# Kernel tuning notes

Measured on AMD Instinct MI355X. Metric: run time of the kernel, lower is better.

The kernel has to match this reference:

```python
import jax, jax.numpy as jnp
import numpy as np

B = 1 << 20  # batch rows
H = 2        # LSTM input_size = hidden_size = 2
K = 11       # number of parallel LSTMs
C = 34       # classifier input size (11*2 + 12 others)
C15 = 51     # int(34 * 1.5)
P = 5        # toPredict_size


def setup_inputs() -> dict:
    key = jax.random.key(0)
    ks = jax.random.split(key, 12)
    s = 0.1
    inp = {
        "input_data": jax.random.normal(ks[0], (B, C), dtype=jnp.float32),
        # Per-LSTM input->gates weights, PyTorch gate order (i, f, g, o): [K, 4H, H]
        "W_ih": jax.random.normal(ks[1], (K, 4 * H, H), dtype=jnp.float32) * s,
        "b_ih": jax.random.normal(ks[2], (K, 4 * H), dtype=jnp.float32) * s,
        # h0 = 0 so W_hh contributes nothing; only its bias b_hh matters.
        "b_hh": jax.random.normal(ks[3], (K, 4 * H), dtype=jnp.float32) * s,
        "W1": jax.random.normal(ks[4], (C15, C), dtype=jnp.float32) * s,
        "b1": jax.random.normal(ks[5], (C15,), dtype=jnp.float32) * s,
        "W2": jax.random.normal(ks[6], (C15, C15), dtype=jnp.float32) * s,
        "b2": jax.random.normal(ks[7], (C15,), dtype=jnp.float32) * s,
        "W3": jax.random.normal(ks[8], (C, C15), dtype=jnp.float32) * s,
        "b3": jax.random.normal(ks[9], (C,), dtype=jnp.float32) * s,
        "W4": jax.random.normal(ks[10], (P, C), dtype=jnp.float32) * s,
        "b4": jax.random.normal(ks[11], (P,), dtype=jnp.float32) * s,
    }
    return inp


def _lstm_heads(x, W_ih, b_ih, b_hh):
    # x: [B, K, H]; single-step LSTM from zero state for each of K heads.
    gates = jnp.einsum("bkh,kgh->bkg", x, W_ih) + b_ih + b_hh  # [B, K, 4H]
    i, f, g, o = jnp.split(gates, 4, axis=-1)  # each [B, K, H]
    c = jax.nn.sigmoid(i) * jnp.tanh(g)        # f*c0 = 0 since c0 = 0
    h = jax.nn.sigmoid(o) * jnp.tanh(c)
    return h  # [B, K, H]


def reference(input_data, W_ih, b_ih, b_hh, W1, b1, W2, b2, W3, b3, W4, b4):
    bsz = input_data.shape[0]
    x_seqs = input_data[:, : K * H].reshape(bsz, K, H)
    others = input_data[:, K * H :]  # [B, 12]
    h = _lstm_heads(x_seqs, W_ih, b_ih, b_hh).reshape(bsz, K * H)
    cated = jnp.concatenate([h, others], axis=-1)  # [B, 34]
    z = jax.nn.relu(cated @ W1.T + b1)
    z = jax.nn.relu(z @ W2.T + b2)
    z = jax.nn.relu(z @ W3.T + b3)
    out = jax.nn.sigmoid(z @ W4.T + b4)  # [B, 5]
    return out
```

## Files before the change

### kernel.cpp

```cpp
#include <hip/hip_runtime.h>


#define BLK  256
#define WPB  4
#define KSEQ 11

typedef _Float16 h2   __attribute__((ext_vector_type(2)));
typedef _Float16 h8   __attribute__((ext_vector_type(8)));
typedef float    f4   __attribute__((ext_vector_type(4)));
typedef unsigned u16v __attribute__((ext_vector_type(16)));

struct __attribute__((packed, aligned(8))) pf4 { f4 v; };

#define N_FRAG_U32 6144
#define N_BIAS     3072
#define N_LSTM     288

__device__ __align__(16) float    g_lstm[N_LSTM];
__device__ __align__(16) unsigned g_frag[N_FRAG_U32];
__device__ __align__(16) float    g_bias[N_BIAS];

__device__ __forceinline__ h2 pk(float a, float b) {
    auto r = __builtin_amdgcn_cvt_pkrtz(a, b);
    union { decltype(r) f; h2 h; } c; c.f = r; return c.h;
}
__device__ __forceinline__ unsigned as_u32(h2 h) {
    union { h2 h; unsigned u; } c; c.h = h; return c.u;
}
__device__ __forceinline__ float uf(unsigned u) {
    union { unsigned u; float f; } c; c.u = u; return c.f;
}
__device__ __forceinline__ unsigned pkrelu(float a, float b) {
    h2 p = pk(a, b);
    h2 z = {(_Float16)0.0f, (_Float16)0.0f};
    h2 r = __builtin_elementwise_max(p, z);
    return as_u32(r);
}
__device__ __forceinline__ float fast_exp(float x) {
#if __has_builtin(__builtin_amdgcn_exp2f)
    return __builtin_amdgcn_exp2f(x * 1.44269504088896340736f);
#else
    return __expf(x);
#endif
}
__device__ __forceinline__ float fast_rcp(float x) {
#if __has_builtin(__builtin_amdgcn_rcpf)
    return __builtin_amdgcn_rcpf(x);
#else
    return 1.0f / x;
#endif
}
__device__ __forceinline__ float sig1(float x)  { return fast_rcp(1.0f + fast_exp(-x)); }

__device__ __forceinline__ float sigtanh(float a, float b) {
    float ea = fast_exp(-a);
    float eb = fast_exp(2.0f * b);
    return (eb - 1.0f) * fast_rcp((1.0f + ea) * (eb + 1.0f));
}

__device__ __forceinline__ void sload3(const unsigned* p, u16v& c0, u16v& c1, u16v& c2) {
    asm volatile("s_load_dwordx16 %0, %3, 0x0\n\t"
                 "s_load_dwordx16 %1, %3, 0x40\n\t"
                 "s_load_dwordx16 %2, %3, 0x80\n\t"
                 "s_waitcnt lgkmcnt(0)"
                 : "=&s"(c0), "=&s"(c1), "=&s"(c2) : "s"(p));
}
__device__ __forceinline__ unsigned pick48(const u16v& c0, const u16v& c1, const u16v& c2, int j) {
    return j < 16 ? c0[j] : (j < 32 ? c1[j - 16] : c2[j - 32]);
}

__device__ __forceinline__ void lstm_one(const u16v& c0, const u16v& c1, const u16v& c2, int base,
                                         float2 x, h2& outp)
{
    float w0  = uf(pick48(c0, c1, c2, base + 0)),  w1  = uf(pick48(c0, c1, c2, base + 1));
    float w2  = uf(pick48(c0, c1, c2, base + 2)),  w3  = uf(pick48(c0, c1, c2, base + 3));
    float w8  = uf(pick48(c0, c1, c2, base + 8)),  w9  = uf(pick48(c0, c1, c2, base + 9));
    float w10 = uf(pick48(c0, c1, c2, base + 10)), w11 = uf(pick48(c0, c1, c2, base + 11));
    float w12 = uf(pick48(c0, c1, c2, base + 12)), w13 = uf(pick48(c0, c1, c2, base + 13));
    float w14 = uf(pick48(c0, c1, c2, base + 14)), w15 = uf(pick48(c0, c1, c2, base + 15));
    float B0  = uf(pick48(c0, c1, c2, base + 16)), B1v = uf(pick48(c0, c1, c2, base + 17));
    float B4  = uf(pick48(c0, c1, c2, base + 20)), B5  = uf(pick48(c0, c1, c2, base + 21));
    float B6  = uf(pick48(c0, c1, c2, base + 22)), B7  = uf(pick48(c0, c1, c2, base + 23));

    float x0 = x.x, x1 = x.y;
    float gi0 = B0  + x0 * w0  + x1 * w1;
    float gi1 = B1v + x0 * w2  + x1 * w3;
    float gg0 = B4  + x0 * w8  + x1 * w9;
    float gg1 = B5  + x0 * w10 + x1 * w11;
    float go0 = B6  + x0 * w12 + x1 * w13;
    float go1 = B7  + x0 * w14 + x1 * w15;
    float cc0 = sigtanh(gi0, gg0);
    float cc1 = sigtanh(gi1, gg1);
    float h0  = sigtanh(go0, cc0);
    float h1  = sigtanh(go1, cc1);
    outp = pk(h0, h1);
}

__global__ void prep_weights(const float* __restrict__ W_ih, const float* __restrict__ b_ih,
                             const float* __restrict__ b_hh,
                             const float* __restrict__ W1, const float* __restrict__ b1,
                             const float* __restrict__ W2, const float* __restrict__ b2,
                             const float* __restrict__ W3, const float* __restrict__ b3,
                             const float* __restrict__ W4, const float* __restrict__ b4)
{
    const int gid = blockIdx.x * blockDim.x + threadIdx.x;
    const int gs  = gridDim.x * blockDim.x;

    for (int i = gid; i < N_FRAG_U32; i += gs) {
        int t = i >> 8, rlo = i & 255;
        int lane = rlo >> 2, j = rlo & 3;
        const float* W; int N, K, ld, ks, nt;
        if (t < 8)       { W = W1; N = 51; K = 34; ld = 34; ks = t >> 2;     nt = t & 3; }
        else if (t < 16) { W = W2; N = 51; K = 51; ld = 51; ks = (t-8) >> 2; nt = (t-8) & 3; }
        else if (t < 22) { W = W3; N = 34; K = 51; ld = 51; ks = (t-16) / 3; nt = (t-16) % 3; }
        else             { W = W4; N = 5;  K = 34; ld = 34; ks = t - 22;     nt = 0; }
        int m = nt * 16 + (lane & 15);
        int k_lo, k_hi;
        if (t < 8) {
            int p = ks * 16 + (lane >> 4) * 4 + j;
            k_lo = 2 * p; k_hi = k_lo + 1;
        } else {
            int q = ks * 32 + (lane >> 4) * 8 + 2 * j;
            k_lo = (2 * (q >> 5) + ((q & 7) >> 2)) * 16 + ((q >> 3) & 3) * 4 + (q & 3);
            int q1 = q + 1;
            k_hi = (2 * (q1 >> 5) + ((q1 & 7) >> 2)) * 16 + ((q1 >> 3) & 3) * 4 + (q1 & 3);
        }
        float a = (m < N && k_lo < K) ? W[m * ld + k_lo] : 0.f;
        float b = (m < N && k_hi < K) ? W[m * ld + k_hi] : 0.f;
        g_frag[i] = as_u32(pk(a, b));
    }
    for (int i = gid; i < N_BIAS; i += gs) {
        int bt = i >> 8, rem = i & 255;
        int lane = rem >> 2, r = rem & 3;
        const float* bv; int N, ot;
        if (bt < 4)       { bv = b1; N = 51; ot = bt; }
        else if (bt < 8)  { bv = b2; N = 51; ot = bt - 4; }
        else if (bt < 11) { bv = b3; N = 34; ot = bt - 8; }
        else              { bv = b4; N = 5;  ot = 0; }
        int n = ot * 16 + (lane >> 4) * 4 + r;
        g_bias[i] = (n < N) ? bv[n] : 0.f;
    }
    for (int i = gid; i < N_LSTM; i += gs) {
        int k = i / 24, cc = i - k * 24;
        float v = 0.f;
        if (k < KSEQ) v = (cc < 16) ? W_ih[k * 16 + cc]
                                    : b_ih[k * 8 + (cc - 16)] + b_hh[k * 8 + (cc - 16)];
        g_lstm[i] = v;
    }
}

__device__ __forceinline__ h8 load_frag(int tile, int l) {
    union { uint4 u; h8 h; } u;
    u.u = *(const uint4*)&g_frag[tile * 256 + l * 4];
    return u.h;
}

__device__ __forceinline__ void read_bfrags(h8 (&bf)[4][2], const unsigned* my, int l)
{
    const int c = l & 15, g = l >> 4;
    const int mrd = (c & 7) << 2;
    #pragma unroll
    for (int st = 0; st < 4; ++st)
      #pragma unroll
      for (int ks = 0; ks < 2; ++ks) {
        int idx = (st * 16 + c) * 32 + ((ks * 16 + g * 4) ^ mrd);
        union { uint4 u; h8 h; } u;
        u.u = *(const uint4*)&my[idx];
        bf[st][ks] = u.h;
      }
}

template<int NT, int TBASE, int BBASE>
__device__ __forceinline__ void layer_swapped(const h8 (&bf)[4][2], f4 (&acc)[4][4], int l)
{
    #pragma unroll
    for (int ot = 0; ot < NT; ++ot) {
        f4 bias4 = *(const f4*)&g_bias[(BBASE + ot) * 256 + l * 4];
        h8 af = load_frag(TBASE + ot, l);
        #pragma unroll
        for (int st = 0; st < 4; ++st)
          acc[ot][st] = __builtin_amdgcn_mfma_f32_16x16x32_f16(af, bf[st][0], bias4, 0, 0, 0);
    }
    #pragma unroll
    for (int ot = 0; ot < NT; ++ot) {
        h8 af = load_frag(TBASE + NT + ot, l);
        #pragma unroll
        for (int st = 0; st < 4; ++st)
          acc[ot][st] = __builtin_amdgcn_mfma_f32_16x16x32_f16(af, bf[st][1], acc[ot][st], 0, 0, 0);
    }
}

template<int NT>
__device__ __forceinline__ void pack_bfrags(const f4 (&acc)[4][4], h8 (&bf)[4][2])
{
    #pragma unroll
    for (int st = 0; st < 4; ++st)
      #pragma unroll
      for (int ks = 0; ks < 2; ++ks) {
        const int o0 = 2 * ks, o1 = 2 * ks + 1;
        union { unsigned u[4]; h8 h; } cvt;
        cvt.u[0] = pkrelu(acc[o0][st][0], acc[o0][st][1]);
        cvt.u[1] = pkrelu(acc[o0][st][2], acc[o0][st][3]);
        if (o1 < NT) {
            cvt.u[2] = pkrelu(acc[o1][st][0], acc[o1][st][1]);
            cvt.u[3] = pkrelu(acc[o1][st][2], acc[o1][st][3]);
        } else {
            cvt.u[2] = 0u; cvt.u[3] = 0u;
        }
        bf[st][ks] = cvt.h;
      }
}

__device__ __forceinline__ void stage0(const unsigned (&cp)[32], unsigned* my, int l)
{
    const int m = (l & 7) << 2;
    #pragma unroll
    for (int ch = 0; ch < 8; ++ch) {
        uint4 q = make_uint4(cp[4*ch], cp[4*ch+1], cp[4*ch+2], cp[4*ch+3]);
        *(uint4*)&my[l * 32 + ((4 * ch) ^ m)] = q;
    }
}

__global__ __launch_bounds__(BLK, 3)
void fused_rnn_mlp(const float* __restrict__ in, float* __restrict__ out, int nrows)
{
    __shared__ unsigned act[WPB * 2048];
    const int tid = threadIdx.x;
    const int w = tid >> 6, l = tid & 63;
    unsigned* my = &act[w * 2048];
    const long long rb = (long long)blockIdx.x * BLK;
    if (rb + BLK > nrows) return;
    const long long rw = rb + w * 64;

    float2 x[17];
    {
        const float* rp = in + (rw + l) * 34;
        #pragma unroll
        for (int q = 0; q < 8; ++q) {
            f4 v = ((const pf4*)(rp))[q].v;
            x[2 * q]     = make_float2(v.x, v.y);
            x[2 * q + 1] = make_float2(v.z, v.w);
        }
        x[16] = *(const float2*)(rp + 32);
    }

    unsigned cp[32];
    #pragma unroll
    for (int kp = 0; kp < 6; ++kp) {
        u16v c0, c1, c2;
        sload3((const unsigned*)&g_lstm[kp * 48], c0, c1, c2);
        h2 h;
        lstm_one(c0, c1, c2, 0, x[2 * kp], h);
        cp[2 * kp] = as_u32(h);
        if (kp < 5) {
            lstm_one(c0, c1, c2, 24, x[2 * kp + 1], h);
            cp[2 * kp + 1] = as_u32(h);
        }
    }
    #pragma unroll
    for (int t = 0; t < 6; ++t) cp[11 + t] = as_u32(pk(x[11 + t].x, x[11 + t].y));
    #pragma unroll
    for (int t = 17; t < 32; ++t) cp[t] = 0u;

    stage0(cp, my, l);

    h8 bf[4][2];
    f4 acc[4][4];

    read_bfrags(bf, my, l);
    layer_swapped<4, 0, 0>(bf, acc, l);
    pack_bfrags<4>(acc, bf);
    layer_swapped<4, 8, 4>(bf, acc, l);
    pack_bfrags<4>(acc, bf);
    layer_swapped<3, 16, 8>(bf, acc, l);
    pack_bfrags<3>(acc, bf);
    layer_swapped<1, 22, 11>(bf, acc, l);

    {
        const int c = l & 15, g = l >> 4;
        float* po = (float*)my;
        #pragma unroll
        for (int st = 0; st < 4; ++st) {
            const int sample = st * 16 + c;
            #pragma unroll
            for (int r = 0; r < 4; ++r) {
                int n = g * 4 + r;
                if (n < 5) po[sample * 9 + n] = acc[0][st][r];
            }
        }
    }

    {
        const float* po = (const float*)my;
        const long long ob = rw * 5;
        #pragma unroll
        for (int it = 0; it < 5; ++it) {
            int F   = it * 64 + l;
            int row = (F * 52429) >> 18;
            int cc  = F - row * 5;
            out[ob + F] = sig1(po[row * 9 + cc]);
        }
    }
}

extern "C" void kernel_launch(void* const* d_in, const int* in_sizes, int n_in,
                              void* d_out, int out_size, void* d_ws, size_t ws_size,
                              hipStream_t stream)
{
    const float* input = (const float*)d_in[0];
    const float* W_ih  = (const float*)d_in[1];
    const float* b_ih  = (const float*)d_in[2];
    const float* b_hh  = (const float*)d_in[3];
    const float* W1    = (const float*)d_in[4];
    const float* b1    = (const float*)d_in[5];
    const float* W2    = (const float*)d_in[6];
    const float* b2    = (const float*)d_in[7];
    const float* W3    = (const float*)d_in[8];
    const float* b3    = (const float*)d_in[9];
    const float* W4    = (const float*)d_in[10];
    const float* b4    = (const float*)d_in[11];
    float* out = (float*)d_out;

    int nrows = in_sizes[0] / 34;
    int grid  = nrows / BLK;

    hipLaunchKernelGGL(prep_weights, dim3(8), dim3(256), 0, stream,
                       W_ih, b_ih, b_hh, W1, b1, W2, b2, W3, b3, W4, b4);
    hipLaunchKernelGGL(fused_rnn_mlp, dim3(grid), dim3(BLK), 0, stream,
                       input, out, nrows);
}
```

Before: 53.02 us.

## Compute LSTM gate preactivations with MFMA and process samples in two halves

The per-head LSTM gate dot products, previously done with scalar FMAs using weights loaded into SGPRs, are moved into an augmented 112-row MFMA layer. That layer also passes the 12 extra features through an identity block. The first MLP layer's fragment mapping is permuted to match the new packed hidden layout. The wave's 64 samples are now processed in two halves of 32 to cut accumulator register pressure. This trades scalar VALU work for extra MFMA work, which mostly multiplies zeros, and sends the LSTM inputs through fp16 before the gate math, which may reduce accuracy.

```diff
diff --git a/kernel.cpp b/kernel.cpp
--- a/kernel.cpp
+++ b/kernel.cpp
@@ -3,20 +3,27 @@
 
 #define BLK  256
 #define WPB  4
-#define KSEQ 11
-
-typedef _Float16 h2   __attribute__((ext_vector_type(2)));
-typedef _Float16 h8   __attribute__((ext_vector_type(8)));
-typedef float    f4   __attribute__((ext_vector_type(4)));
-typedef unsigned u16v __attribute__((ext_vector_type(16)));
+
+#define N_FRAG_U32 (38 * 256)
+#define N_BIAS     (19 * 256)
+
+#define TB_G  0
+#define TB_L1 14
+#define TB_L2 22
+#define TB_L3 30
+#define TB_L4 36
+#define BB_L1 0
+#define BB_L2 4
+#define BB_L3 8
+#define BB_L4 11
+#define BB_G  12
+
+typedef _Float16 h2 __attribute__((ext_vector_type(2)));
+typedef _Float16 h8 __attribute__((ext_vector_type(8)));
+typedef float    f4 __attribute__((ext_vector_type(4)));
 
 struct __attribute__((packed, aligned(8))) pf4 { f4 v; };
 
-#define N_FRAG_U32 6144
-#define N_BIAS     3072
-#define N_LSTM     288
-
-__device__ __align__(16) float    g_lstm[N_LSTM];
 __device__ __align__(16) unsigned g_frag[N_FRAG_U32];
 __device__ __align__(16) float    g_bias[N_BIAS];
 
@@ -50,50 +57,43 @@
     return 1.0f / x;
 #endif
 }
-__device__ __forceinline__ float sig1(float x)  { return fast_rcp(1.0f + fast_exp(-x)); }
-
+__device__ __forceinline__ float sig1(float x) { return fast_rcp(1.0f + fast_exp(-x)); }
 __device__ __forceinline__ float sigtanh(float a, float b) {
     float ea = fast_exp(-a);
     float eb = fast_exp(2.0f * b);
     return (eb - 1.0f) * fast_rcp((1.0f + ea) * (eb + 1.0f));
 }
 
-__device__ __forceinline__ void sload3(const unsigned* p, u16v& c0, u16v& c1, u16v& c2) {
-    asm volatile("s_load_dwordx16 %0, %3, 0x0\n\t"
-                 "s_load_dwordx16 %1, %3, 0x40\n\t"
-                 "s_load_dwordx16 %2, %3, 0x80\n\t"
-                 "s_waitcnt lgkmcnt(0)"
-                 : "=&s"(c0), "=&s"(c1), "=&s"(c2) : "s"(p));
-}
-__device__ __forceinline__ unsigned pick48(const u16v& c0, const u16v& c1, const u16v& c2, int j) {
-    return j < 16 ? c0[j] : (j < 32 ? c1[j - 16] : c2[j - 32]);
-}
-
-__device__ __forceinline__ void lstm_one(const u16v& c0, const u16v& c1, const u16v& c2, int base,
-                                         float2 x, h2& outp)
-{
-    float w0  = uf(pick48(c0, c1, c2, base + 0)),  w1  = uf(pick48(c0, c1, c2, base + 1));
-    float w2  = uf(pick48(c0, c1, c2, base + 2)),  w3  = uf(pick48(c0, c1, c2, base + 3));
-    float w8  = uf(pick48(c0, c1, c2, base + 8)),  w9  = uf(pick48(c0, c1, c2, base + 9));
-    float w10 = uf(pick48(c0, c1, c2, base + 10)), w11 = uf(pick48(c0, c1, c2, base + 11));
-    float w12 = uf(pick48(c0, c1, c2, base + 12)), w13 = uf(pick48(c0, c1, c2, base + 13));
-    float w14 = uf(pick48(c0, c1, c2, base + 14)), w15 = uf(pick48(c0, c1, c2, base + 15));
-    float B0  = uf(pick48(c0, c1, c2, base + 16)), B1v = uf(pick48(c0, c1, c2, base + 17));
-    float B4  = uf(pick48(c0, c1, c2, base + 20)), B5  = uf(pick48(c0, c1, c2, base + 21));
-    float B6  = uf(pick48(c0, c1, c2, base + 22)), B7  = uf(pick48(c0, c1, c2, base + 23));
-
-    float x0 = x.x, x1 = x.y;
-    float gi0 = B0  + x0 * w0  + x1 * w1;
-    float gi1 = B1v + x0 * w2  + x1 * w3;
-    float gg0 = B4  + x0 * w8  + x1 * w9;
-    float gg1 = B5  + x0 * w10 + x1 * w11;
-    float go0 = B6  + x0 * w12 + x1 * w13;
-    float go1 = B7  + x0 * w14 + x1 * w15;
-    float cc0 = sigtanh(gi0, gg0);
-    float cc1 = sigtanh(gi1, gg1);
-    float h0  = sigtanh(go0, cc0);
-    float h1  = sigtanh(go1, cc1);
-    outp = pk(h0, h1);
+__device__ __forceinline__ int pi_map(int q) {
+    return (2 * (q >> 5) + ((q & 7) >> 2)) * 16 + ((q >> 3) & 3) * 4 + (q & 3);
+}
+__device__ __forceinline__ int phi_map(int q) {
+    int ksq = q >> 5, rem = q & 31, gq = rem >> 3, jj = rem & 7;
+    if (ksq == 0) {
+        if (jj < 6) { int u = 4 * jj + gq; return (u < 22) ? u : -1; }
+        return (gq < 3) ? (22 + 4 * gq + (jj - 6)) : -1;
+    }
+    if (jj < 2 && gq < 3) return 24 + 4 * gq + jj;
+    return -1;
+}
+__device__ __forceinline__ float waug(int row, int feat, const float* W_ih) {
+    if (feat >= 34) return 0.f;
+    if (row >= 96) { int cf = row - 96; return (cf < 12 && feat == 22 + cf) ? 1.f : 0.f; }
+    int u = row >> 2, r = row & 3;
+    if (u >= 22 || r == 3) return 0.f;
+    int k = u >> 1, jg = u & 1;
+    if ((feat >> 1) != k) return 0.f;
+    int h = feat & 1;
+    int g8 = (r == 0) ? jg : (r == 1) ? 4 + jg : 6 + jg;
+    return W_ih[k * 16 + g8 * 2 + h];
+}
+__device__ __forceinline__ float baug(int row, const float* b_ih, const float* b_hh) {
+    if (row >= 96) return 0.f;
+    int u = row >> 2, r = row & 3;
+    if (u >= 22 || r == 3) return 0.f;
+    int k = u >> 1, jg = u & 1;
+    int g8 = (r == 0) ? jg : (r == 1) ? 4 + jg : 6 + jg;
+    return b_ih[k * 8 + g8] + b_hh[k * 8 + g8];
 }
 
 __global__ void prep_weights(const float* __restrict__ W_ih, const float* __restrict__ b_ih,
@@ -109,43 +109,51 @@
     for (int i = gid; i < N_FRAG_U32; i += gs) {
         int t = i >> 8, rlo = i & 255;
         int lane = rlo >> 2, j = rlo & 3;
-        const float* W; int N, K, ld, ks, nt;
-        if (t < 8)       { W = W1; N = 51; K = 34; ld = 34; ks = t >> 2;     nt = t & 3; }
-        else if (t < 16) { W = W2; N = 51; K = 51; ld = 51; ks = (t-8) >> 2; nt = (t-8) & 3; }
-        else if (t < 22) { W = W3; N = 34; K = 51; ld = 51; ks = (t-16) / 3; nt = (t-16) % 3; }
-        else             { W = W4; N = 5;  K = 34; ld = 34; ks = t - 22;     nt = 0; }
-        int m = nt * 16 + (lane & 15);
-        int k_lo, k_hi;
-        if (t < 8) {
+        float a, b;
+        if (t < TB_L1) {
+            int ks = t / 7, ot = t - ks * 7;
+            int row = ot * 16 + (lane & 15);
             int p = ks * 16 + (lane >> 4) * 4 + j;
-            k_lo = 2 * p; k_hi = k_lo + 1;
+            a = waug(row, 2 * p,     W_ih);
+            b = waug(row, 2 * p + 1, W_ih);
         } else {
-            int q = ks * 32 + (lane >> 4) * 8 + 2 * j;
-            k_lo = (2 * (q >> 5) + ((q & 7) >> 2)) * 16 + ((q >> 3) & 3) * 4 + (q & 3);
-            int q1 = q + 1;
-            k_hi = (2 * (q1 >> 5) + ((q1 & 7) >> 2)) * 16 + ((q1 >> 3) & 3) * 4 + (q1 & 3);
-        }
-        float a = (m < N && k_lo < K) ? W[m * ld + k_lo] : 0.f;
-        float b = (m < N && k_hi < K) ? W[m * ld + k_hi] : 0.f;
+            const float* W; int N, K, ld, ks, nt, usephi;
+            if (t < TB_L2)      { W = W1; N = 51; K = 34; ld = 34; int tt = t - TB_L1; ks = tt >> 2; nt = tt & 3; usephi = 1; }
+            else if (t < TB_L3) { W = W2; N = 51; K = 51; ld = 51; int tt = t - TB_L2; ks = tt >> 2; nt = tt & 3; usephi = 0; }
+            else if (t < TB_L4) { W = W3; N = 34; K = 51; ld = 51; int tt = t - TB_L3; ks = tt / 3; nt = tt - 3 * ks; usephi = 0; }
+            else                { W = W4; N = 5;  K = 34; ld = 34; ks = t - TB_L4; nt = 0; usephi = 0; }
+            int m  = nt * 16 + (lane & 15);
+            int q0 = ks * 32 + (lane >> 4) * 8 + 2 * j;
+            int f0, f1;
+            if (usephi) { f0 = phi_map(q0); f1 = phi_map(q0 + 1); }
+            else {
+                f0 = pi_map(q0);     if (f0 >= K) f0 = -1;
+                f1 = pi_map(q0 + 1); if (f1 >= K) f1 = -1;
+            }
+            a = (m < N && f0 >= 0) ? W[m * ld + f0] : 0.f;
+            b = (m < N && f1 >= 0) ? W[m * ld + f1] : 0.f;
+        }
         g_frag[i] = as_u32(pk(a, b));
     }
+
     for (int i = gid; i < N_BIAS; i += gs) {
         int bt = i >> 8, rem = i & 255;
         int lane = rem >> 2, r = rem & 3;
-        const float* bv; int N, ot;
-        if (bt < 4)       { bv = b1; N = 51; ot = bt; }
-        else if (bt < 8)  { bv = b2; N = 51; ot = bt - 4; }
-        else if (bt < 11) { bv = b3; N = 34; ot = bt - 8; }
-        else              { bv = b4; N = 5;  ot = 0; }
-        int n = ot * 16 + (lane >> 4) * 4 + r;
-        g_bias[i] = (n < N) ? bv[n] : 0.f;
-    }
-    for (int i = gid; i < N_LSTM; i += gs) {
-        int k = i / 24, cc = i - k * 24;
-        float v = 0.f;
-        if (k < KSEQ) v = (cc < 16) ? W_ih[k * 16 + cc]
-                                    : b_ih[k * 8 + (cc - 16)] + b_hh[k * 8 + (cc - 16)];
-        g_lstm[i] = v;
+        int rowloc = (lane >> 4) * 4 + r;
+        float v;
+        if (bt < BB_G) {
+            const float* bv; int N, ot;
+            if (bt < 4)       { bv = b1; N = 51; ot = bt; }
+            else if (bt < 8)  { bv = b2; N = 51; ot = bt - 4; }
+            else if (bt < 11) { bv = b3; N = 34; ot = bt - 8; }
+            else              { bv = b4; N = 5;  ot = 0; }
+            int n = ot * 16 + rowloc;
+            v = (n < N) ? bv[n] : 0.f;
+        } else {
+            int row = (bt - BB_G) * 16 + rowloc;
+            v = baug(row, b_ih, b_hh);
+        }
+        g_bias[i] = v;
     }
 }
 
@@ -155,46 +163,77 @@
     return u.h;
 }
 
-__device__ __forceinline__ void read_bfrags(h8 (&bf)[4][2], const unsigned* my, int l)
-{
+__device__ __forceinline__ void read_bfrags2(h8 (&bf)[2][2], const unsigned* my, int l, int half) {
     const int c = l & 15, g = l >> 4;
     const int mrd = (c & 7) << 2;
     #pragma unroll
-    for (int st = 0; st < 4; ++st)
+    for (int st = 0; st < 2; ++st)
       #pragma unroll
       for (int ks = 0; ks < 2; ++ks) {
-        int idx = (st * 16 + c) * 32 + ((ks * 16 + g * 4) ^ mrd);
+        int idx = ((half * 2 + st) * 16 + c) * 32 + ((ks * 16 + g * 4) ^ mrd);
         union { uint4 u; h8 h; } u;
         u.u = *(const uint4*)&my[idx];
         bf[st][ks] = u.h;
       }
 }
 
+__device__ __forceinline__ void layer_gates(const h8 (&bf)[2][2], f4 (&acc)[7][2], int l) {
+    #pragma unroll
+    for (int ot = 0; ot < 7; ++ot) {
+        f4 bias4 = *(const f4*)&g_bias[(BB_G + ot) * 256 + l * 4];
+        h8 af = load_frag(TB_G + ot, l);
+        acc[ot][0] = __builtin_amdgcn_mfma_f32_16x16x32_f16(af, bf[0][0], bias4, 0, 0, 0);
+        acc[ot][1] = __builtin_amdgcn_mfma_f32_16x16x32_f16(af, bf[1][0], bias4, 0, 0, 0);
+    }
+    #pragma unroll
+    for (int ot = 0; ot < 7; ++ot) {
+        h8 af = load_frag(TB_G + 7 + ot, l);
+        acc[ot][0] = __builtin_amdgcn_mfma_f32_16x16x32_f16(af, bf[0][1], acc[ot][0], 0, 0, 0);
+        acc[ot][1] = __builtin_amdgcn_mfma_f32_16x16x32_f16(af, bf[1][1], acc[ot][1], 0, 0, 0);
+    }
+}
+
+__device__ __forceinline__ void gates_to_bf(const f4 (&acc)[7][2], h8 (&bf)[2][2]) {
+    #pragma unroll
+    for (int st = 0; st < 2; ++st) {
+        float h[6];
+        #pragma unroll
+        for (int ot = 0; ot < 6; ++ot) {
+            float cc = sigtanh(acc[ot][st][0], acc[ot][st][1]);
+            h[ot]    = sigtanh(acc[ot][st][2], cc);
+        }
+        union { unsigned u[4]; h8 hh; } c0, c1;
+        c0.u[0] = as_u32(pk(h[0], h[1]));
+        c0.u[1] = as_u32(pk(h[2], h[3]));
+        c0.u[2] = as_u32(pk(h[4], h[5]));
+        c0.u[3] = as_u32(pk(acc[6][st][0], acc[6][st][1]));
+        c1.u[0] = as_u32(pk(acc[6][st][2], acc[6][st][3]));
+        c1.u[1] = 0u; c1.u[2] = 0u; c1.u[3] = 0u;
+        bf[st][0] = c0.hh; bf[st][1] = c1.hh;
+    }
+}
+
 template<int NT, int TBASE, int BBASE>
-__device__ __forceinline__ void layer_swapped(const h8 (&bf)[4][2], f4 (&acc)[4][4], int l)
-{
+__device__ __forceinline__ void layerN(const h8 (&bf)[2][2], f4 (&acc)[4][2], int l) {
     #pragma unroll
     for (int ot = 0; ot < NT; ++ot) {
         f4 bias4 = *(const f4*)&g_bias[(BBASE + ot) * 256 + l * 4];
         h8 af = load_frag(TBASE + ot, l);
-        #pragma unroll
-        for (int st = 0; st < 4; ++st)
-          acc[ot][st] = __builtin_amdgcn_mfma_f32_16x16x32_f16(af, bf[st][0], bias4, 0, 0, 0);
+        acc[ot][0] = __builtin_amdgcn_mfma_f32_16x16x32_f16(af, bf[0][0], bias4, 0, 0, 0);
+        acc[ot][1] = __builtin_amdgcn_mfma_f32_16x16x32_f16(af, bf[1][0], bias4, 0, 0, 0);
     }
     #pragma unroll
     for (int ot = 0; ot < NT; ++ot) {
         h8 af = load_frag(TBASE + NT + ot, l);
-        #pragma unroll
-        for (int st = 0; st < 4; ++st)
-          acc[ot][st] = __builtin_amdgcn_mfma_f32_16x16x32_f16(af, bf[st][1], acc[ot][st], 0, 0, 0);
+        acc[ot][0] = __builtin_amdgcn_mfma_f32_16x16x32_f16(af, bf[0][1], acc[ot][0], 0, 0, 0);
+        acc[ot][1] = __builtin_amdgcn_mfma_f32_16x16x32_f16(af, bf[1][1], acc[ot][1], 0, 0, 0);
     }
 }
 
 template<int NT>
-__device__ __forceinline__ void pack_bfrags(const f4 (&acc)[4][4], h8 (&bf)[4][2])
-{
-    #pragma unroll
-    for (int st = 0; st < 4; ++st)
+__device__ __forceinline__ void pack_bfrags2(const f4 (&acc)[4][2], h8 (&bf)[2][2]) {
+    #pragma unroll
+    for (int st = 0; st < 2; ++st)
       #pragma unroll
       for (int ks = 0; ks < 2; ++ks) {
         const int o0 = 2 * ks, o1 = 2 * ks + 1;
@@ -211,8 +250,7 @@
       }
 }
 
-__device__ __forceinline__ void stage0(const unsigned (&cp)[32], unsigned* my, int l)
-{
+__device__ __forceinline__ void stage0(const unsigned (&cp)[32], unsigned* my, int l) {
     const int m = (l & 7) << 2;
     #pragma unroll
     for (int ch = 0; ch < 8; ++ch) {
@@ -232,64 +270,58 @@
     if (rb + BLK > nrows) return;
     const long long rw = rb + w * 64;
 
-    float2 x[17];
+    unsigned cp[32];
     {
         const float* rp = in + (rw + l) * 34;
         #pragma unroll
         for (int q = 0; q < 8; ++q) {
             f4 v = ((const pf4*)(rp))[q].v;
-            x[2 * q]     = make_float2(v.x, v.y);
-            x[2 * q + 1] = make_float2(v.z, v.w);
-        }
-        x[16] = *(const float2*)(rp + 32);
-    }
-
-    unsigned cp[32];
-    #pragma unroll
-    for (int kp = 0; kp < 6; ++kp) {
-        u16v c0, c1, c2;
-        sload3((const unsigned*)&g_lstm[kp * 48], c0, c1, c2);
-        h2 h;
-        lstm_one(c0, c1, c2, 0, x[2 * kp], h);
-        cp[2 * kp] = as_u32(h);
-        if (kp < 5) {
-            lstm_one(c0, c1, c2, 24, x[2 * kp + 1], h);
-            cp[2 * kp + 1] = as_u32(h);
-        }
-    }
-    #pragma unroll
-    for (int t = 0; t < 6; ++t) cp[11 + t] = as_u32(pk(x[11 + t].x, x[11 + t].y));
-    #pragma unroll
-    for (int t = 17; t < 32; ++t) cp[t] = 0u;
-
+            cp[2 * q]     = as_u32(pk(v.x, v.y));
+            cp[2 * q + 1] = as_u32(pk(v.z, v.w));
+        }
+        float2 t = *(const float2*)(rp + 32);
+        cp[16] = as_u32(pk(t.x, t.y));
+        #pragma unroll
+        for (int t2 = 17; t2 < 32; ++t2) cp[t2] = 0u;
+    }
     stage0(cp, my, l);
 
-    h8 bf[4][2];
-    f4 acc[4][4];
-
-    read_bfrags(bf, my, l);
-    layer_swapped<4, 0, 0>(bf, acc, l);
-    pack_bfrags<4>(acc, bf);
-    layer_swapped<4, 8, 4>(bf, acc, l);
-    pack_bfrags<4>(acc, bf);
-    layer_swapped<3, 16, 8>(bf, acc, l);
-    pack_bfrags<3>(acc, bf);
-    layer_swapped<1, 22, 11>(bf, acc, l);
+    f4 outh[2][2];
+
+    #pragma unroll
+    for (int half = 0; half < 2; ++half) {
+        h8 bf[2][2];
+        read_bfrags2(bf, my, l, half);
+
+        f4 accg[7][2];
+        layer_gates(bf, accg, l);
+        gates_to_bf(accg, bf);
+
+        f4 acc[4][2];
+        layerN<4, TB_L1, BB_L1>(bf, acc, l);
+        pack_bfrags2<4>(acc, bf);
+        layerN<4, TB_L2, BB_L2>(bf, acc, l);
+        pack_bfrags2<4>(acc, bf);
+        layerN<3, TB_L3, BB_L3>(bf, acc, l);
+        pack_bfrags2<3>(acc, bf);
+        layerN<1, TB_L4, BB_L4>(bf, acc, l);
+        outh[half][0] = acc[0][0];
+        outh[half][1] = acc[0][1];
+    }
 
     {
         const int c = l & 15, g = l >> 4;
         float* po = (float*)my;
         #pragma unroll
-        for (int st = 0; st < 4; ++st) {
-            const int sample = st * 16 + c;
+        for (int hs = 0; hs < 4; ++hs) {
+            const int sample = hs * 16 + c;
             #pragma unroll
             for (int r = 0; r < 4; ++r) {
                 int n = g * 4 + r;
-                if (n < 5) po[sample * 9 + n] = acc[0][st][r];
+                if (n < 5) po[sample * 9 + n] = outh[hs >> 1][hs & 1][r];
             }
         }
     }
-
     {
         const float* po = (const float*)my;
         const long long ob = rw * 5;
```

Result: slower. 77.56 us (+46.3%).
